# Kernel optimization log

Hardware: AMD Instinct MI355X
Metric: run time of the kernel (lower is better)

## Reference

```python
import jax, jax.numpy as jnp
import numpy as np

B, S, E, H, L, OUT = 128, 256, 300, 512, 2, 2


def _lstm_dir(x, mask, w_ih, w_hh, b, h0, c0, reverse):
    """One direction of one LSTM layer with length masking (packed-seq semantics).
    x: [B,S,D], mask: [B,S] bool (t < length). Returns (outputs [B,S,H], final h [B,H]).
    For reverse=True, scan runs t=S-1..0; state only updates once t < length, which
    exactly reproduces pack_padded_sequence reverse-direction behavior.
    """
    def step(carry, inp):
        h, c = carry
        xt, mt = inp  # [B,D], [B]
        z = xt @ w_ih.T + h @ w_hh.T + b  # [B,4H], torch gate order i,f,g,o
        i, f, g, o = jnp.split(z, 4, axis=-1)
        c_new = jax.nn.sigmoid(f) * c + jax.nn.sigmoid(i) * jnp.tanh(g)
        h_new = jax.nn.sigmoid(o) * jnp.tanh(c_new)
        m = mt[:, None]
        h = jnp.where(m, h_new, h)
        c = jnp.where(m, c_new, c)
        return (h, c), h
    (hT, _), hs = jax.lax.scan(step, (h0, c0), (jnp.swapaxes(x, 0, 1), mask.T), reverse=reverse)
    return jnp.swapaxes(hs, 0, 1), hT


def setup_inputs():
    key = jax.random.key(0)
    ks = iter(jax.random.split(key, 32))
    lengths = jax.random.randint(next(ks), (B,), 1, S + 1)
    x = jax.random.normal(next(ks), (B, S, E), jnp.float32)
    # module encodes per-sample lengths in input[:, -1, 0]
    x = x.at[:, -1, 0].set(lengths.astype(jnp.float32))
    k = 1.0 / np.sqrt(H)
    def u(shape):
        return jax.random.uniform(next(ks), shape, jnp.float32, -k, k)
    d = {"x": x}
    for l in range(L):
        din = E if l == 0 else 2 * H
        for suf in ("f", "r"):
            d[f"w_ih_l{l}_{suf}"] = u((4 * H, din))
            d[f"w_hh_l{l}_{suf}"] = u((4 * H, H))
            d[f"b_ih_l{l}_{suf}"] = u((4 * H,))
            d[f"b_hh_l{l}_{suf}"] = u((4 * H,))
    d["fc1_w"] = u((H, H))
    d["fc1_b"] = u((H,))
    d["fc_w"] = u((OUT, H))
    d["fc_b"] = u((OUT,))
    return d


def _forward(x, params):
    Bx, Sx = x.shape[0], x.shape[1]
    lengths = jnp.minimum(x[:, -1, 0].astype(jnp.int32), Sx)  # clamp(max=seq_len)
    mask = jnp.arange(Sx)[None, :] < lengths[:, None]  # [B,S]
    h0 = jnp.ones((Bx, H), x.dtype)  # module uses ones, not zeros
    c0 = jnp.ones((Bx, H), x.dtype)
    inp = x
    hT_r = None
    for l in range(L):
        (wif, whf, bif, bhf), (wir, whr, bir, bhr) = params[l]
        out_f, _ = _lstm_dir(inp, mask, wif, whf, bif + bhf, h0, c0, False)
        out_r, hT_r = _lstm_dir(inp, mask, wir, whr, bir + bhr, h0, c0, True)
        inp = jnp.concatenate([out_f, out_r], axis=-1)  # [B,S,2H]
    # ht[-1] == final hidden of reverse direction of last layer
    return hT_r


def reference(x, w_ih_l0_f, w_hh_l0_f, b_ih_l0_f, b_hh_l0_f,
              w_ih_l0_r, w_hh_l0_r, b_ih_l0_r, b_hh_l0_r,
              w_ih_l1_f, w_hh_l1_f, b_ih_l1_f, b_hh_l1_f,
              w_ih_l1_r, w_hh_l1_r, b_ih_l1_r, b_hh_l1_r,
              fc1_w, fc1_b, fc_w, fc_b):
    params = [((w_ih_l0_f, w_hh_l0_f, b_ih_l0_f, b_hh_l0_f),
               (w_ih_l0_r, w_hh_l0_r, b_ih_l0_r, b_hh_l0_r)),
              ((w_ih_l1_f, w_hh_l1_f, b_ih_l1_f, b_hh_l1_f),
               (w_ih_l1_r, w_hh_l1_r, b_ih_l1_r, b_hh_l1_r))]
    ht = _forward(x, params)  # [B,H]
    out = ht @ fc1_w.T + fc1_b  # fc1 (no activation in original)
    return out @ fc_w.T + fc_b  # [B,OUT]
```

## Files before the change

### kernel.cpp

```cpp
#include <hip/hip_runtime.h>

#define B_  128
#define S_  256
#define E_  300
#define EP_ 320
#define H_  512
#define G_  2048
#define D1_ 1024
#define G2_ 4096
#define FSLOT_ 4
#define FA_WORDS_ (4*FSLOT_*4*32*32)
#define FC_WORDS_ (2*FSLOT_*4*32*32)

typedef _Float16 f16;
typedef __attribute__((ext_vector_type(8))) _Float16 f16x8;
typedef __attribute__((ext_vector_type(4))) float    f32x4;
typedef unsigned long long u64;
typedef unsigned int u32;

__device__ __forceinline__ float sigf(float x){ return 1.f/(1.f + __expf(-x)); }
__device__ __forceinline__ float tanhf_(float x){
  float e = __expf(-2.f*fabsf(x));
  float t = (1.f - e)/(1.f + e);
  return x < 0.f ? -t : t;
}

__device__ __forceinline__ u64 aload64(const u64* p){
  return __hip_atomic_load((u64*)p, __ATOMIC_RELAXED, __HIP_MEMORY_SCOPE_AGENT);
}
__device__ __forceinline__ u32 aload32(const u32* p){
  return __hip_atomic_load((u32*)p, __ATOMIC_RELAXED, __HIP_MEMORY_SCOPE_AGENT);
}
__device__ __forceinline__ void astore32(u32* p, u32 v){
  __hip_atomic_store(p, v, __ATOMIC_RELAXED, __HIP_MEMORY_SCOPE_AGENT);
}
union H8 { u64 q[2]; f16x8 v; };
union FU { f16 f; unsigned short s; };


__global__ void k_f32_to_f16(const float* __restrict__ s, f16* __restrict__ d, int n){
  int i = blockIdx.x*blockDim.x + threadIdx.x;
  if (i < n) d[i] = (f16)s[i];
}

__global__ void k_pad_w(const float* __restrict__ s, f16* __restrict__ d, int rows, int ks, int kd){
  int i = blockIdx.x*blockDim.x + threadIdx.x;
  if (i >= rows*kd) return;
  int r = i/kd, k = i - r*kd;
  d[i] = (k < ks) ? (f16)s[(size_t)r*ks + k] : (f16)0.f;
}

__global__ void k_cast_x(const float* __restrict__ x, f16* __restrict__ xf){
  int i = blockIdx.x*blockDim.x + threadIdx.x;
  if (i >= S_*B_*EP_) return;
  int e = i % EP_; int rm = i / EP_;
  int m = rm % B_; int t = rm / B_;
  xf[i] = (e < E_) ? (f16)x[((size_t)m*S_ + t)*E_ + e] : (f16)0.f;
}

__global__ void k_bias(const float* __restrict__ a, const float* __restrict__ b,
                       float* __restrict__ d, int n){
  int i = blockIdx.x*blockDim.x + threadIdx.x;
  if (i < n) d[i] = a[i] + b[i];
}

__global__ void k_len(const float* __restrict__ x, int* __restrict__ len){
  int b = threadIdx.x;
  if (b < B_){
    int v = (int)x[((size_t)b*S_ + (S_-1))*E_];
    len[b] = v > S_ ? S_ : v;
  }
}

__global__ void k_zero(u32* __restrict__ p, int n){
  int i = blockIdx.x*blockDim.x + threadIdx.x;
  if (i < n) p[i] = 0u;
}

__global__ void k_init(f16* hxA, f16* hx1, float* cstate){
  int i = blockIdx.x*blockDim.x + threadIdx.x;
  if (i < B_*H_){
    hxA[i] = (f16)1.f;
    hxA[2*B_*H_ + i] = (f16)1.f;
    hx1[i] = (f16)1.f;
    cstate[i] = 1.f;
  }
}


__global__ __launch_bounds__(256) void k_gemm_bt(
    const f16* __restrict__ A, const f16* __restrict__ Bm,
    f16* __restrict__ C, const float* __restrict__ bias,
    int M, int N, int K)
{
  __shared__ f16 As[128*32];
  __shared__ f16 Bs[128*32];
  const int m0 = blockIdx.x*128, n0 = blockIdx.y*128;
  const int tid = threadIdx.x;
  const int w = tid>>6, lane = tid&63, quad = lane>>4, l16 = lane&15;
  const int wm = (w&1)*64, wn = (w>>1)*64;
  const int srow = w*32 + (lane>>2);
  const int scol = (lane&3)*8;
  const f16* Ap  = A  + (size_t)(m0 + srow)*K + scol;
  const f16* Bp  = Bm + (size_t)(n0 + srow)*K + scol;
  const f16* Ap2 = Ap + (size_t)16*K;
  const f16* Bp2 = Bp + (size_t)16*K;
  f16* ldsA  = &As[(w*32)*32];
  f16* ldsA2 = &As[(w*32+16)*32];
  f16* ldsB  = &Bs[(w*32)*32];
  f16* ldsB2 = &Bs[(w*32+16)*32];
  f32x4 z4 = {0.f,0.f,0.f,0.f};
  f32x4 acc[4][4];
#pragma unroll
  for (int mi = 0; mi < 4; ++mi)
#pragma unroll
    for (int ni = 0; ni < 4; ++ni) acc[mi][ni] = z4;

  for (int k0 = 0; k0 < K; k0 += 32){
    __builtin_amdgcn_global_load_lds(
        (const __attribute__((address_space(1))) void*)(Ap + k0),
        (__attribute__((address_space(3))) void*)ldsA, 16, 0, 0);
    __builtin_amdgcn_global_load_lds(
        (const __attribute__((address_space(1))) void*)(Ap2 + k0),
        (__attribute__((address_space(3))) void*)ldsA2, 16, 0, 0);
    __builtin_amdgcn_global_load_lds(
        (const __attribute__((address_space(1))) void*)(Bp + k0),
        (__attribute__((address_space(3))) void*)ldsB, 16, 0, 0);
    __builtin_amdgcn_global_load_lds(
        (const __attribute__((address_space(1))) void*)(Bp2 + k0),
        (__attribute__((address_space(3))) void*)ldsB2, 16, 0, 0);
    asm volatile("s_waitcnt vmcnt(0)" ::: "memory");
    __syncthreads();
    f16x8 a[4], b[4];
#pragma unroll
    for (int mi = 0; mi < 4; ++mi)
      a[mi] = *(const f16x8*)&As[(wm + mi*16 + l16)*32 + quad*8];
#pragma unroll
    for (int ni = 0; ni < 4; ++ni)
      b[ni] = *(const f16x8*)&Bs[(wn + ni*16 + l16)*32 + quad*8];
#pragma unroll
    for (int mi = 0; mi < 4; ++mi)
#pragma unroll
      for (int ni = 0; ni < 4; ++ni)
        acc[mi][ni] = __builtin_amdgcn_mfma_f32_16x16x32_f16(a[mi], b[ni], acc[mi][ni],0,0,0);
    __syncthreads();
  }
#pragma unroll
  for (int mi = 0; mi < 4; ++mi)
#pragma unroll
    for (int ni = 0; ni < 4; ++ni){
      int col = n0 + wn + ni*16 + l16;
      float bz = bias[col];
#pragma unroll
      for (int r = 0; r < 4; ++r){
        int row = m0 + wm + mi*16 + quad*4 + r;
        C[(size_t)row*N + col] = (f16)(acc[mi][ni][r] + bz);
      }
    }
}


__global__ __launch_bounds__(256, 1) void k_phaseA(
    const float* __restrict__ x, const f16* __restrict__ xz,
    const f16* __restrict__ w0f, const f16* __restrict__ w0r,
    const f16* __restrict__ whf, const f16* __restrict__ whr,
    const float* __restrict__ bs0, const int* __restrict__ len,
    f16* __restrict__ hxA, f16* __restrict__ outcat,
    u32* __restrict__ flagsA)
{
  __shared__ f16 Wh[64*512];
  __shared__ f16 Wi[64*320];
  const int half = blockIdx.x, jb = blockIdx.y, dir = blockIdx.z;
  const f16* wih = dir ? w0r : w0f;
  const f16* whh = dir ? whr : whf;
  const float* bias = bs0 + dir*G_;
  f16* hx = hxA + (size_t)dir*(2*B_*H_);
  u32* fbase = flagsA + (size_t)(dir*2 + half)*(FSLOT_*4*32*32);
  const int tid = threadIdx.x;
  const int w = tid>>6, lane = tid&63, quad = lane>>4, l16 = lane&15;
  const int j0 = jb*16;
  const int m0 = half*64 + w*16;

  for (int u = tid; u < 4096; u += 256){
    int lrr = u>>6, uc = u&63;
    int g = lrr>>4, i = lrr&15;
    *(uint4*)&Wh[lrr*512 + (uc ^ (i&7))*8] =
        *(const uint4*)(whh + ((size_t)(g*H_ + j0 + i))*H_ + uc*8);
  }
  if (!xz){
    for (int u = tid; u < 2560; u += 256){
      int row = u/40, c = u - row*40;
      int g = row>>4, i = row&15;
      *(uint4*)&Wi[row*320 + (c ^ (i&7))*8] =
          *(const uint4*)(wih + ((size_t)(g*H_ + j0 + i))*EP_ + c*8);
    }
  }
  __syncthreads();

  const int j = j0 + l16;
  float bz[4], hprev[4], cpr[4]; int lm[4];
#pragma unroll
  for (int g = 0; g < 4; ++g) bz[g] = bias[g*H_ + j];
#pragma unroll
  for (int r = 0; r < 4; ++r){ hprev[r] = 1.f; cpr[r] = 1.f; lm[r] = len[m0 + quad*4 + r]; }
  const size_t xrowbase = (size_t)(m0 + l16)*S_;

  if (xz){
    for (int s = 0; s < S_; ++s){
      const int t = dir ? (S_-1-s) : s;

      const f16* zr = xz + ((size_t)t*B_)*G2_ + dir*G_;
      float zvv[4][4];
#pragma unroll
      for (int g = 0; g < 4; ++g)
#pragma unroll
        for (int r = 0; r < 4; ++r)
          zvv[g][r] = (float)zr[(size_t)(m0 + quad*4 + r)*G2_ + g*H_ + j];

      if (s > 0){
        const u32* fp = fbase + ((size_t)((s-1)&(FSLOT_-1))*4 + w)*32*32;
        const u32 expv = (u32)s;
        for (;;){
          u32 v = aload32(fp + (size_t)(lane & 31)*32);
          if (__ballot(v == expv) == ~0ull) break;
        }
        asm volatile("" ::: "memory");
      }

      const int par = s & 1;
      const u64* hap = (const u64*)(hx + (size_t)par*(B_*H_) + (size_t)(m0 + l16)*H_);
      f32x4 z4 = {0.f,0.f,0.f,0.f};
      f32x4 acc[4] = {z4,z4,z4,z4};
      u64 hq[32];
#pragma unroll
      for (int kb = 0; kb < 16; ++kb){
        hq[2*kb]   = aload64(hap + kb*8 + quad*2);
        hq[2*kb+1] = aload64(hap + kb*8 + quad*2 + 1);
      }
#pragma unroll
      for (int kb = 0; kb < 16; ++kb){
        H8 ha;
        ha.q[0] = hq[2*kb];
        ha.q[1] = hq[2*kb+1];
        int uq = kb*4 + quad;
#pragma unroll
        for (int g = 0; g < 4; ++g){
          f16x8 b = *(const f16x8*)&Wh[(g*16+l16)*512 + ((uq ^ (l16&7)))*8];
          acc[g] = __builtin_amdgcn_mfma_f32_16x16x32_f16(ha.v, b, acc[g],0,0,0);
        }
      }

      f16* hn = hx + (size_t)(1-par)*(B_*H_);
#pragma unroll
      for (int r = 0; r < 4; ++r){
        int m = m0 + quad*4 + r;
        float zi = acc[0][r] + zvv[0][r];
        float zf = acc[1][r] + zvv[1][r];
        float zg = acc[2][r] + zvv[2][r];
        float zo = acc[3][r] + zvv[3][r];
        float ig = sigf(zi), fg = sigf(zf), gg = tanhf_(zg), og = sigf(zo);
        float cnew = fg*cpr[r] + ig*gg;
        float hnew = og*tanhf_(cnew);
        bool mk = t < lm[r];
        float hsel = mk ? hnew : hprev[r];
        cpr[r] = mk ? cnew : cpr[r];
        hprev[r] = hsel;
        FU cv; cv.f = (f16)hsel;
        int other = __shfl_down((int)cv.s, 1);
        if ((l16 & 1) == 0)
          astore32((u32*)(hn + (size_t)m*H_ + j), (u32)cv.s | ((u32)other << 16));
      }
      asm volatile("s_waitcnt vmcnt(0)" ::: "memory");
      if (lane == 0)
        astore32(fbase + (((size_t)(s&(FSLOT_-1))*4 + w)*32 + jb)*32, (u32)(s+1));

#pragma unroll
      for (int r = 0; r < 4; ++r){
        int m = m0 + quad*4 + r;
        FU cv; cv.f = (f16)hprev[r];
        int other = __shfl_down((int)cv.s, 1);
        if ((l16 & 1) == 0)
          *(u32*)(outcat + ((size_t)t*B_ + m)*D1_ + dir*H_ + j) = (u32)cv.s | ((u32)other << 16);
      }
    }
    return;
  }

  float4 xA[9], xB[9]; float xT[8];
  {
    const int t0 = dir ? (S_-1) : 0;
    const float* xr = x + (xrowbase + t0)*E_;
#pragma unroll
    for (int kb = 0; kb < 9; ++kb){
      xA[kb] = *(const float4*)(xr + kb*32 + quad*8);
      xB[kb] = *(const float4*)(xr + kb*32 + quad*8 + 4);
    }
    int kbase = 288 + quad*8;
#pragma unroll
    for (int e2 = 0; e2 < 8; ++e2)
      xT[e2] = (kbase + e2 < E_) ? xr[kbase + e2] : 0.f;
  }

  for (int s = 0; s < S_; ++s){
    const int t = dir ? (S_-1-s) : s;
    f32x4 z4 = {0.f,0.f,0.f,0.f};
    f32x4 acc[4] = {z4,z4,z4,z4};

#pragma unroll
    for (int kb = 0; kb < 9; ++kb){
      f16x8 a;
      a[0]=(f16)xA[kb].x; a[1]=(f16)xA[kb].y; a[2]=(f16)xA[kb].z; a[3]=(f16)xA[kb].w;
      a[4]=(f16)xB[kb].x; a[5]=(f16)xB[kb].y; a[6]=(f16)xB[kb].z; a[7]=(f16)xB[kb].w;
      int c = (kb*4 + quad) ^ (l16 & 7);
#pragma unroll
      for (int g = 0; g < 4; ++g){
        f16x8 b = *(const f16x8*)&Wi[(g*16+l16)*320 + c*8];
        acc[g] = __builtin_amdgcn_mfma_f32_16x16x32_f16(a, b, acc[g],0,0,0);
      }
    }
    {
      f16x8 a;
#pragma unroll
      for (int e2 = 0; e2 < 8; ++e2) a[e2] = (f16)xT[e2];
      int c = (36 + quad) ^ (l16 & 7);
#pragma unroll
      for (int g = 0; g < 4; ++g){
        f16x8 b = *(const f16x8*)&Wi[(g*16+l16)*320 + c*8];
        acc[g] = __builtin_amdgcn_mfma_f32_16x16x32_f16(a, b, acc[g],0,0,0);
      }
    }

    if (s+1 < S_){
      const int tn = dir ? (S_-2-s) : (s+1);
      const float* xr = x + (xrowbase + tn)*E_;
#pragma unroll
      for (int kb = 0; kb < 9; ++kb){
        xA[kb] = *(const float4*)(xr + kb*32 + quad*8);
        xB[kb] = *(const float4*)(xr + kb*32 + quad*8 + 4);
      }
      int kbase = 288 + quad*8;
#pragma unroll
      for (int e2 = 0; e2 < 8; ++e2)
        xT[e2] = (kbase + e2 < E_) ? xr[kbase + e2] : 0.f;
    }

    if (s > 0){
      const u32* fp = fbase + ((size_t)((s-1)&(FSLOT_-1))*4 + w)*32*32;
      const u32 expv = (u32)s;
      for (;;){
        u32 v = aload32(fp + (size_t)(lane & 31)*32);
        if (__ballot(v == expv) == ~0ull) break;
      }
      asm volatile("" ::: "memory");
    }

    const int par = s & 1;
    const u64* hap = (const u64*)(hx + (size_t)par*(B_*H_) + (size_t)(m0 + l16)*H_);
    u64 hq[32];
#pragma unroll
    for (int kb = 0; kb < 16; ++kb){
      hq[2*kb]   = aload64(hap + kb*8 + quad*2);
      hq[2*kb+1] = aload64(hap + kb*8 + quad*2 + 1);
    }
#pragma unroll
    for (int kb = 0; kb < 16; ++kb){
      H8 ha;
      ha.q[0] = hq[2*kb];
      ha.q[1] = hq[2*kb+1];
      int uq = kb*4 + quad;
#pragma unroll
      for (int g = 0; g < 4; ++g){
        f16x8 b = *(const f16x8*)&Wh[(g*16+l16)*512 + ((uq ^ (l16&7)))*8];
        acc[g] = __builtin_amdgcn_mfma_f32_16x16x32_f16(ha.v, b, acc[g],0,0,0);
      }
    }

    f16* hn = hx + (size_t)(1-par)*(B_*H_);
#pragma unroll
    for (int r = 0; r < 4; ++r){
      int m = m0 + quad*4 + r;
      float zi = acc[0][r] + bz[0];
      float zf = acc[1][r] + bz[1];
      float zg = acc[2][r] + bz[2];
      float zo = acc[3][r] + bz[3];
      float ig = sigf(zi), fg = sigf(zf), gg = tanhf_(zg), og = sigf(zo);
      float cnew = fg*cpr[r] + ig*gg;
      float hnew = og*tanhf_(cnew);
      bool mk = t < lm[r];
      float hsel = mk ? hnew : hprev[r];
      cpr[r] = mk ? cnew : cpr[r];
      hprev[r] = hsel;
      FU cv; cv.f = (f16)hsel;
      int other = __shfl_down((int)cv.s, 1);
      if ((l16 & 1) == 0)
        astore32((u32*)(hn + (size_t)m*H_ + j), (u32)cv.s | ((u32)other << 16));
    }
    asm volatile("s_waitcnt vmcnt(0)" ::: "memory");
    if (lane == 0)
      astore32(fbase + (((size_t)(s&(FSLOT_-1))*4 + w)*32 + jb)*32, (u32)(s+1));

#pragma unroll
    for (int r = 0; r < 4; ++r){
      int m = m0 + quad*4 + r;
      FU cv; cv.f = (f16)hprev[r];
      int other = __shfl_down((int)cv.s, 1);
      if ((l16 & 1) == 0)
        *(u32*)(outcat + ((size_t)t*B_ + m)*D1_ + dir*H_ + j) = (u32)cv.s | ((u32)other << 16);
    }
  }
}


__global__ __launch_bounds__(256, 1) void k_phaseCrec(
    const f16* __restrict__ Z1c, const f16* __restrict__ w1h,
    const int* __restrict__ len,
    f16* __restrict__ hx1, float* __restrict__ cstate, float* __restrict__ h1f,
    u32* __restrict__ flagsC, int s0, int CH)
{
  __shared__ f16 Wh[64*512];
  const int half = blockIdx.x, jb = blockIdx.y;
  u32* fbase = flagsC + (size_t)half*(FSLOT_*4*32*32);
  const int tid = threadIdx.x;
  const int w = tid>>6, lane = tid&63, quad = lane>>4, l16 = lane&15;
  const int j0 = jb*16;
  const int m0 = half*64 + w*16;

  for (int u = tid; u < 4096; u += 256){
    int lrr = u>>6, uc = u&63;
    int g = lrr>>4, i = lrr&15;
    *(uint4*)&Wh[lrr*512 + (uc ^ (i&7))*8] =
        *(const uint4*)(w1h + ((size_t)(g*H_ + j0 + i))*H_ + uc*8);
  }
  __syncthreads();

  const int j = j0 + l16;
  float hprev[4], cpr[4]; int lm[4];
#pragma unroll
  for (int r = 0; r < 4; ++r){
    int m = m0 + quad*4 + r;
    lm[r] = len[m];
    cpr[r] = cstate[(size_t)m*H_ + j];
    hprev[r] = (float)hx1[(size_t)(s0 & 1)*(B_*H_) + (size_t)m*H_ + j];
  }

  for (int sl = 0; sl < CH; ++sl){
    const int s = s0 + sl;
    const int t = S_-1-s;
    const int zrow = CH-1-sl;

    float zv[4][4];
#pragma unroll
    for (int g = 0; g < 4; ++g)
#pragma unroll
      for (int r = 0; r < 4; ++r)
        zv[g][r] = (float)Z1c[((size_t)zrow*B_ + m0 + quad*4 + r)*G_ + g*H_ + j];

    if (s > 0){
      const u32* fp = fbase + ((size_t)((s-1)&(FSLOT_-1))*4 + w)*32*32;
      const u32 expv = (u32)s;
      for (;;){
        u32 v = aload32(fp + (size_t)(lane & 31)*32);
        if (__ballot(v == expv) == ~0ull) break;
      }
      asm volatile("" ::: "memory");
    }

    const int par = s & 1;
    const u64* hap = (const u64*)(hx1 + (size_t)par*(B_*H_) + (size_t)(m0 + l16)*H_);
    f32x4 z4 = {0.f,0.f,0.f,0.f};
    f32x4 acc[4] = {z4,z4,z4,z4};
    u64 hq[32];
#pragma unroll
    for (int kb = 0; kb < 16; ++kb){
      hq[2*kb]   = aload64(hap + kb*8 + quad*2);
      hq[2*kb+1] = aload64(hap + kb*8 + quad*2 + 1);
    }
#pragma unroll
    for (int kb = 0; kb < 16; ++kb){
      H8 ha;
      ha.q[0] = hq[2*kb];
      ha.q[1] = hq[2*kb+1];
      int uq = kb*4 + quad;
#pragma unroll
      for (int g = 0; g < 4; ++g){
        f16x8 b = *(const f16x8*)&Wh[(g*16+l16)*512 + ((uq ^ (l16&7)))*8];
        acc[g] = __builtin_amdgcn_mfma_f32_16x16x32_f16(ha.v, b, acc[g],0,0,0);
      }
    }

    f16* hn = hx1 + (size_t)(1-par)*(B_*H_);
#pragma unroll
    for (int r = 0; r < 4; ++r){
      int m = m0 + quad*4 + r;
      float zi = acc[0][r] + zv[0][r];
      float zf = acc[1][r] + zv[1][r];
      float zg = acc[2][r] + zv[2][r];
      float zo = acc[3][r] + zv[3][r];
      float ig = sigf(zi), fg = sigf(zf), gg = tanhf_(zg), og = sigf(zo);
      float cnew = fg*cpr[r] + ig*gg;
      float hnew = og*tanhf_(cnew);
      bool mk = t < lm[r];
      float hsel = mk ? hnew : hprev[r];
      cpr[r] = mk ? cnew : cpr[r];
      hprev[r] = hsel;
      FU cv; cv.f = (f16)hsel;
      int other = __shfl_down((int)cv.s, 1);
      if ((l16 & 1) == 0)
        astore32((u32*)(hn + (size_t)m*H_ + j), (u32)cv.s | ((u32)other << 16));
    }
    asm volatile("s_waitcnt vmcnt(0)" ::: "memory");
    if (lane == 0)
      astore32(fbase + (((size_t)(s&(FSLOT_-1))*4 + w)*32 + jb)*32, (u32)(s+1));

    if (t == 0){
#pragma unroll
      for (int r = 0; r < 4; ++r)
        h1f[(size_t)(m0 + quad*4 + r)*H_ + j] = hprev[r];
    }
  }

#pragma unroll
  for (int r = 0; r < 4; ++r)
    cstate[(size_t)(m0 + quad*4 + r)*H_ + j] = cpr[r];
}


__global__ void k_fold(const float* __restrict__ fc1w, const float* __restrict__ fc1b,
                       const float* __restrict__ fcw,  const float* __restrict__ fcb,
                       float* __restrict__ Mf, float* __restrict__ bf){
  int i = blockIdx.x*blockDim.x + threadIdx.x;
  if (i >= 1024) return;
  int o = i >> 9, h = i & 511;
  float s = 0.f;
  for (int jj = 0; jj < 512; ++jj) s += fcw[o*512 + jj] * fc1w[jj*512 + h];
  Mf[o*512 + h] = s;
  if (h == 0){
    float sb = fcb[o];
    for (int jj = 0; jj < 512; ++jj) sb += fcw[o*512 + jj] * fc1b[jj];
    bf[o] = sb;
  }
}

__global__ void k_final(const float* __restrict__ h1f, const float* __restrict__ Mf,
                        const float* __restrict__ bf, float* __restrict__ out){
  int i = threadIdx.x;
  if (i >= 256) return;
  int b = i >> 1, o = i & 1;
  float s = bf[o];
  const float* hp = h1f + (size_t)b*512;
  const float* mp = Mf + (size_t)o*512;
  for (int h = 0; h < 512; ++h) s += hp[h]*mp[h];
  out[b*2 + o] = s;
}


extern "C" void kernel_launch(void* const* d_in, const int* in_sizes, int n_in,
                              void* d_out, int out_size, void* d_ws, size_t ws_size,
                              hipStream_t stream)
{
  const float* x     = (const float*)d_in[0];
  const float* wih0f = (const float*)d_in[1];
  const float* whh0f = (const float*)d_in[2];
  const float* bih0f = (const float*)d_in[3];
  const float* bhh0f = (const float*)d_in[4];
  const float* wih0r = (const float*)d_in[5];
  const float* whh0r = (const float*)d_in[6];
  const float* bih0r = (const float*)d_in[7];
  const float* bhh0r = (const float*)d_in[8];
  const float* wih1r = (const float*)d_in[13];
  const float* whh1r = (const float*)d_in[14];
  const float* bih1r = (const float*)d_in[15];
  const float* bhh1r = (const float*)d_in[16];
  const float* fc1w  = (const float*)d_in[17];
  const float* fc1b  = (const float*)d_in[18];
  const float* fcw   = (const float*)d_in[19];
  const float* fcb   = (const float*)d_in[20];
  float* out = (float*)d_out;

  char* p = (char*)d_ws;
  auto alloc = [&](size_t bytes)->char*{
    char* r = p; p += (bytes + 255) & ~(size_t)255; return r;
  };
  f16* w0fp   = (f16*)alloc((size_t)G_*EP_*2);
  f16* w0rp   = (f16*)alloc((size_t)G_*EP_*2);
  f16* whf    = (f16*)alloc((size_t)G_*H_*2);
  f16* whr    = (f16*)alloc((size_t)G_*H_*2);
  f16* w1i    = (f16*)alloc((size_t)G_*D1_*2);
  f16* w1h    = (f16*)alloc((size_t)G_*H_*2);
  float* bs0  = (float*)alloc((size_t)2*G_*4);
  float* bs1r = (float*)alloc(G_*4);
  int*   len  = (int*)alloc(B_*4);
  f16* outcat = (f16*)alloc((size_t)S_*B_*D1_*2);
  f16* hxA    = (f16*)alloc((size_t)2*2*B_*H_*2);
  f16* hx1    = (f16*)alloc((size_t)2*B_*H_*2);
  float* cstate=(float*)alloc((size_t)B_*H_*4);
  float* h1f  = (float*)alloc((size_t)B_*H_*4);
  float* Mf   = (float*)alloc(2*512*4);
  float* bf   = (float*)alloc(256);
  u32* flagsA = (u32*)alloc((size_t)FA_WORDS_*4);
  u32* flagsC = (u32*)alloc((size_t)FC_WORDS_*4);
  size_t used = (size_t)(p - (char*)d_ws);

  const size_t XZ_BYTES = (size_t)S_*B_*G2_*2;
  const size_t XF_BYTES = (size_t)S_*B_*EP_*2;
  f16* Xz = nullptr; f16* xf = nullptr; f16* Z1c; int CH;
  if (used + XZ_BYTES + XF_BYTES + 512 <= ws_size){
    Xz  = (f16*)alloc(XZ_BYTES);
    xf  = (f16*)alloc(XF_BYTES);
    Z1c = Xz;
    CH  = 256;
  } else {
    CH = 8;
    for (int c = 256; c >= 8; c >>= 1){
      if (used + (size_t)c*B_*G_*2 <= ws_size){ CH = c; break; }
    }
    Z1c = (f16*)alloc((size_t)CH*B_*G_*2);
  }
  const int NC = S_/CH;

  int n;
  n = G_*EP_; k_pad_w<<<(n+255)/256, 256, 0, stream>>>(wih0f, w0fp, G_, E_, EP_);
              k_pad_w<<<(n+255)/256, 256, 0, stream>>>(wih0r, w0rp, G_, E_, EP_);
  n = G_*H_;  k_f32_to_f16<<<(n+255)/256,256,0,stream>>>(whh0f, whf, n);
              k_f32_to_f16<<<(n+255)/256,256,0,stream>>>(whh0r, whr, n);
              k_f32_to_f16<<<(n+255)/256,256,0,stream>>>(whh1r, w1h, n);
  n = G_*D1_; k_f32_to_f16<<<(n+255)/256,256,0,stream>>>(wih1r, w1i, n);
  k_bias<<<8,256,0,stream>>>(bih0f, bhh0f, bs0, G_);
  k_bias<<<8,256,0,stream>>>(bih0r, bhh0r, bs0 + G_, G_);
  k_bias<<<8,256,0,stream>>>(bih1r, bhh1r, bs1r, G_);
  k_len<<<1,128,0,stream>>>(x, len);
  k_init<<<(B_*H_+255)/256,256,0,stream>>>(hxA, hx1, cstate);
  k_zero<<<(FA_WORDS_+255)/256,256,0,stream>>>(flagsA, FA_WORDS_);
  k_zero<<<(FC_WORDS_+255)/256,256,0,stream>>>(flagsC, FC_WORDS_);
  k_fold<<<4,256,0,stream>>>(fc1w, fc1b, fcw, fcb, Mf, bf);

  if (Xz){
    n = S_*B_*EP_;
    k_cast_x<<<(n+255)/256, 256, 0, stream>>>(x, xf);
    k_gemm_bt<<<dim3(S_*B_/128, G2_/128), 256, 0, stream>>>(
        xf, w0fp, Xz, bs0, S_*B_, G2_, EP_);
  }

  k_phaseA<<<dim3(2,32,2), 256, 0, stream>>>(
      x, Xz, w0fp, w0rp, whf, whr, bs0, len, hxA, outcat, flagsA);

  for (int cc = 0; cc < NC; ++cc){
    int t0 = S_ - (cc+1)*CH;
    k_gemm_bt<<<dim3(CH, 16), 256, 0, stream>>>(
        outcat + (size_t)t0*B_*D1_, w1i, Z1c, bs1r, CH*B_, G_, D1_);
    k_phaseCrec<<<dim3(2,32), 256, 0, stream>>>(
        Z1c, w1h, len, hx1, cstate, h1f, flagsC, cc*CH, CH);
  }

  k_final<<<1,256,0,stream>>>(h1f, Mf, bf, out);
}
```

Baseline: 3.971 ms.

## Chunk layer-0 input projection per direction so recurrence fits smaller workspace

Replaces the single combined forward/reverse input-projection GEMM with separate per-direction GEMMs over time chunks sized to the available workspace. A new recurrent kernel consumes each chunk and persists cell and hidden state between launches, so the precomputed-projection path can run even when the full 256-step buffer does not fit. The aim is to avoid falling back to the slower kernel that recomputes the input projection inside the recurrence. In exchange it adds more launches, per-chunk state reload and store, and reloads of recurrent weights into LDS for each chunk.

```diff
diff --git a/kernel.cpp b/kernel.cpp
--- a/kernel.cpp
+++ b/kernel.cpp
@@ -7,7 +7,6 @@
 #define H_  512
 #define G_  2048
 #define D1_ 1024
-#define G2_ 4096
 #define FSLOT_ 4
 #define FA_WORDS_ (4*FSLOT_*4*32*32)
 #define FC_WORDS_ (2*FSLOT_*4*32*32)
@@ -77,13 +76,15 @@
   if (i < n) p[i] = 0u;
 }
 
-__global__ void k_init(f16* hxA, f16* hx1, float* cstate){
+__global__ void k_init(f16* hxA, f16* hx1, float* cstate, float* cstateA){
   int i = blockIdx.x*blockDim.x + threadIdx.x;
   if (i < B_*H_){
     hxA[i] = (f16)1.f;
     hxA[2*B_*H_ + i] = (f16)1.f;
     hx1[i] = (f16)1.f;
     cstate[i] = 1.f;
+    cstateA[i] = 1.f;
+    cstateA[B_*H_ + i] = 1.f;
   }
 }
 
@@ -160,8 +161,132 @@
 }
 
 
+__global__ __launch_bounds__(256, 1) void k_phaseA_xz(
+    const f16* __restrict__ Xzf, const f16* __restrict__ Xzr,
+    const f16* __restrict__ whf, const f16* __restrict__ whr,
+    const int* __restrict__ len,
+    f16* __restrict__ hxA, float* __restrict__ cstateA,
+    f16* __restrict__ outcat, u32* __restrict__ flagsA,
+    int s0, int CHA)
+{
+  __shared__ f16 Wh[64*512];
+  const int half = blockIdx.x, jb = blockIdx.y, dir = blockIdx.z;
+  const f16* whh = dir ? whr : whf;
+  const f16* Xz  = dir ? Xzr : Xzf;
+  f16* hx = hxA + (size_t)dir*(2*B_*H_);
+  float* cst = cstateA + (size_t)dir*(B_*H_);
+  u32* fbase = flagsA + (size_t)(dir*2 + half)*(FSLOT_*4*32*32);
+  const int tid = threadIdx.x;
+  const int w = tid>>6, lane = tid&63, quad = lane>>4, l16 = lane&15;
+  const int j0 = jb*16;
+  const int m0 = half*64 + w*16;
+
+  for (int u = tid; u < 4096; u += 256){
+    int lrr = u>>6, uc = u&63;
+    int g = lrr>>4, i = lrr&15;
+    *(uint4*)&Wh[lrr*512 + (uc ^ (i&7))*8] =
+        *(const uint4*)(whh + ((size_t)(g*H_ + j0 + i))*H_ + uc*8);
+  }
+  __syncthreads();
+
+  const int j = j0 + l16;
+  float hprev[4], cpr[4]; int lm[4];
+#pragma unroll
+  for (int r = 0; r < 4; ++r){
+    int m = m0 + quad*4 + r;
+    lm[r] = len[m];
+    cpr[r] = cst[(size_t)m*H_ + j];
+    hprev[r] = (float)hx[(size_t)(s0 & 1)*(B_*H_) + (size_t)m*H_ + j];
+  }
+
+  for (int sl = 0; sl < CHA; ++sl){
+    const int s = s0 + sl;
+    const int t = dir ? (S_-1-s) : s;
+    const int zrow = dir ? (CHA-1-sl) : sl;
+
+    const f16* zr = Xz + ((size_t)zrow*B_)*G_;
+    float zvv[4][4];
+#pragma unroll
+    for (int g = 0; g < 4; ++g)
+#pragma unroll
+      for (int r = 0; r < 4; ++r)
+        zvv[g][r] = (float)zr[(size_t)(m0 + quad*4 + r)*G_ + g*H_ + j];
+
+    if (s > 0){
+      const u32* fp = fbase + ((size_t)((s-1)&(FSLOT_-1))*4 + w)*32*32;
+      const u32 expv = (u32)s;
+      for (;;){
+        u32 v = aload32(fp + (size_t)(lane & 31)*32);
+        if (__ballot(v == expv) == ~0ull) break;
+      }
+      asm volatile("" ::: "memory");
+    }
+
+    const int par = s & 1;
+    const u64* hap = (const u64*)(hx + (size_t)par*(B_*H_) + (size_t)(m0 + l16)*H_);
+    f32x4 z4 = {0.f,0.f,0.f,0.f};
+    f32x4 acc[4] = {z4,z4,z4,z4};
+    u64 hq[32];
+#pragma unroll
+    for (int kb = 0; kb < 16; ++kb){
+      hq[2*kb]   = aload64(hap + kb*8 + quad*2);
+      hq[2*kb+1] = aload64(hap + kb*8 + quad*2 + 1);
+    }
+#pragma unroll
+    for (int kb = 0; kb < 16; ++kb){
+      H8 ha;
+      ha.q[0] = hq[2*kb];
+      ha.q[1] = hq[2*kb+1];
+      int uq = kb*4 + quad;
+#pragma unroll
+      for (int g = 0; g < 4; ++g){
+        f16x8 b = *(const f16x8*)&Wh[(g*16+l16)*512 + ((uq ^ (l16&7)))*8];
+        acc[g] = __builtin_amdgcn_mfma_f32_16x16x32_f16(ha.v, b, acc[g],0,0,0);
+      }
+    }
+
+    f16* hn = hx + (size_t)(1-par)*(B_*H_);
+#pragma unroll
+    for (int r = 0; r < 4; ++r){
+      int m = m0 + quad*4 + r;
+      float zi = acc[0][r] + zvv[0][r];
+      float zf = acc[1][r] + zvv[1][r];
+      float zg = acc[2][r] + zvv[2][r];
+      float zo = acc[3][r] + zvv[3][r];
+      float ig = sigf(zi), fg = sigf(zf), gg = tanhf_(zg), og = sigf(zo);
+      float cnew = fg*cpr[r] + ig*gg;
+      float hnew = og*tanhf_(cnew);
+      bool mk = t < lm[r];
+      float hsel = mk ? hnew : hprev[r];
+      cpr[r] = mk ? cnew : cpr[r];
+      hprev[r] = hsel;
+      FU cv; cv.f = (f16)hsel;
+      int other = __shfl_down((int)cv.s, 1);
+      if ((l16 & 1) == 0)
+        astore32((u32*)(hn + (size_t)m*H_ + j), (u32)cv.s | ((u32)other << 16));
+    }
+    asm volatile("s_waitcnt vmcnt(0)" ::: "memory");
+    if (lane == 0)
+      astore32(fbase + (((size_t)(s&(FSLOT_-1))*4 + w)*32 + jb)*32, (u32)(s+1));
+
+#pragma unroll
+    for (int r = 0; r < 4; ++r){
+      int m = m0 + quad*4 + r;
+      FU cv; cv.f = (f16)hprev[r];
+      int other = __shfl_down((int)cv.s, 1);
+      if ((l16 & 1) == 0)
+        *(u32*)(outcat + ((size_t)t*B_ + m)*D1_ + dir*H_ + j) = (u32)cv.s | ((u32)other << 16);
+    }
+  }
+
+#pragma unroll
+  for (int r = 0; r < 4; ++r)
+    cst[(size_t)(m0 + quad*4 + r)*H_ + j] = cpr[r];
+}
+
+
 __global__ __launch_bounds__(256, 1) void k_phaseA(
-    const float* __restrict__ x, const f16* __restrict__ xz,
+    const float* __restrict__ x,
     const f16* __restrict__ w0f, const f16* __restrict__ w0r,
     const f16* __restrict__ whf, const f16* __restrict__ whr,
     const float* __restrict__ bs0, const int* __restrict__ len,
@@ -187,13 +312,11 @@
     *(uint4*)&Wh[lrr*512 + (uc ^ (i&7))*8] =
         *(const uint4*)(whh + ((size_t)(g*H_ + j0 + i))*H_ + uc*8);
   }
-  if (!xz){
-    for (int u = tid; u < 2560; u += 256){
-      int row = u/40, c = u - row*40;
-      int g = row>>4, i = row&15;
-      *(uint4*)&Wi[row*320 + (c ^ (i&7))*8] =
-          *(const uint4*)(wih + ((size_t)(g*H_ + j0 + i))*EP_ + c*8);
-    }
+  for (int u = tid; u < 2560; u += 256){
+    int row = u/40, c = u - row*40;
+    int g = row>>4, i = row&15;
+    *(uint4*)&Wi[row*320 + (c ^ (i&7))*8] =
+        *(const uint4*)(wih + ((size_t)(g*H_ + j0 + i))*EP_ + c*8);
   }
   __syncthreads();
 
@@ -204,87 +327,6 @@
 #pragma unroll
   for (int r = 0; r < 4; ++r){ hprev[r] = 1.f; cpr[r] = 1.f; lm[r] = len[m0 + quad*4 + r]; }
   const size_t xrowbase = (size_t)(m0 + l16)*S_;
-
-  if (xz){
-    for (int s = 0; s < S_; ++s){
-      const int t = dir ? (S_-1-s) : s;
-
-      const f16* zr = xz + ((size_t)t*B_)*G2_ + dir*G_;
-      float zvv[4][4];
-#pragma unroll
-      for (int g = 0; g < 4; ++g)
-#pragma unroll
-        for (int r = 0; r < 4; ++r)
-          zvv[g][r] = (float)zr[(size_t)(m0 + quad*4 + r)*G2_ + g*H_ + j];
-
-      if (s > 0){
-        const u32* fp = fbase + ((size_t)((s-1)&(FSLOT_-1))*4 + w)*32*32;
-        const u32 expv = (u32)s;
-        for (;;){
-          u32 v = aload32(fp + (size_t)(lane & 31)*32);
-          if (__ballot(v == expv) == ~0ull) break;
-        }
-        asm volatile("" ::: "memory");
-      }
-
-      const int par = s & 1;
-      const u64* hap = (const u64*)(hx + (size_t)par*(B_*H_) + (size_t)(m0 + l16)*H_);
-      f32x4 z4 = {0.f,0.f,0.f,0.f};
-      f32x4 acc[4] = {z4,z4,z4,z4};
-      u64 hq[32];
-#pragma unroll
-      for (int kb = 0; kb < 16; ++kb){
-        hq[2*kb]   = aload64(hap + kb*8 + quad*2);
-        hq[2*kb+1] = aload64(hap + kb*8 + quad*2 + 1);
-      }
-#pragma unroll
-      for (int kb = 0; kb < 16; ++kb){
-        H8 ha;
-        ha.q[0] = hq[2*kb];
-        ha.q[1] = hq[2*kb+1];
-        int uq = kb*4 + quad;
-#pragma unroll
-        for (int g = 0; g < 4; ++g){
-          f16x8 b = *(const f16x8*)&Wh[(g*16+l16)*512 + ((uq ^ (l16&7)))*8];
-          acc[g] = __builtin_amdgcn_mfma_f32_16x16x32_f16(ha.v, b, acc[g],0,0,0);
-        }
-      }
-
-      f16* hn = hx + (size_t)(1-par)*(B_*H_);
-#pragma unroll
-      for (int r = 0; r < 4; ++r){
-        int m = m0 + quad*4 + r;
-        float zi = acc[0][r] + zvv[0][r];
-        float zf = acc[1][r] + zvv[1][r];
-        float zg = acc[2][r] + zvv[2][r];
-        float zo = acc[3][r] + zvv[3][r];
-        float ig = sigf(zi), fg = sigf(zf), gg = tanhf_(zg), og = sigf(zo);
-        float cnew = fg*cpr[r] + ig*gg;
-        float hnew = og*tanhf_(cnew);
-        bool mk = t < lm[r];
-        float hsel = mk ? hnew : hprev[r];
-        cpr[r] = mk ? cnew : cpr[r];
-        hprev[r] = hsel;
-        FU cv; cv.f = (f16)hsel;
-        int other = __shfl_down((int)cv.s, 1);
-        if ((l16 & 1) == 0)
-          astore32((u32*)(hn + (size_t)m*H_ + j), (u32)cv.s | ((u32)other << 16));
-      }
-      asm volatile("s_waitcnt vmcnt(0)" ::: "memory");
-      if (lane == 0)
-        astore32(fbase + (((size_t)(s&(FSLOT_-1))*4 + w)*32 + jb)*32, (u32)(s+1));
-
-#pragma unroll
-      for (int r = 0; r < 4; ++r){
-        int m = m0 + quad*4 + r;
-        FU cv; cv.f = (f16)hprev[r];
-        int other = __shfl_down((int)cv.s, 1);
-        if ((l16 & 1) == 0)
-          *(u32*)(outcat + ((size_t)t*B_ + m)*D1_ + dir*H_ + j) = (u32)cv.s | ((u32)other << 16);
-      }
-    }
-    return;
-  }
 
   float4 xA[9], xB[9]; float xT[8];
   {
@@ -593,7 +635,8 @@
   f16* outcat = (f16*)alloc((size_t)S_*B_*D1_*2);
   f16* hxA    = (f16*)alloc((size_t)2*2*B_*H_*2);
   f16* hx1    = (f16*)alloc((size_t)2*B_*H_*2);
-  float* cstate=(float*)alloc((size_t)B_*H_*4);
+  float* cstate =(float*)alloc((size_t)B_*H_*4);
+  float* cstateA=(float*)alloc((size_t)2*B_*H_*4);
   float* h1f  = (float*)alloc((size_t)B_*H_*4);
   float* Mf   = (float*)alloc(2*512*4);
   float* bf   = (float*)alloc(256);
@@ -601,20 +644,26 @@
   u32* flagsC = (u32*)alloc((size_t)FC_WORDS_*4);
   size_t used = (size_t)(p - (char*)d_ws);
 
-  const size_t XZ_BYTES = (size_t)S_*B_*G2_*2;
-  const size_t XF_BYTES = (size_t)S_*B_*EP_*2;
-  f16* Xz = nullptr; f16* xf = nullptr; f16* Z1c; int CH;
-  if (used + XZ_BYTES + XF_BYTES + 512 <= ws_size){
-    Xz  = (f16*)alloc(XZ_BYTES);
-    xf  = (f16*)alloc(XF_BYTES);
-    Z1c = Xz;
-    CH  = 256;
+  const size_t XFB = (size_t)S_*B_*EP_*2;
+  const size_t CHUNK1 = (size_t)B_*G_*2;
+  f16* xf = nullptr; f16* Xzf = nullptr; f16* Xzr = nullptr;
+  int CHA = 0;
+  for (int c = 256; c >= 16; c >>= 1){
+    if (used + XFB + 2*(size_t)c*CHUNK1 + 1024 <= ws_size){ CHA = c; break; }
+  }
+  f16* Z1c; int CH;
+  if (CHA){
+    xf  = (f16*)alloc(XFB);
+    Xzf = (f16*)alloc((size_t)CHA*CHUNK1);
+    Xzr = (f16*)alloc((size_t)CHA*CHUNK1);
+    Z1c = Xzf;
+    CH  = (2*CHA > 256) ? 256 : 2*CHA;
   } else {
     CH = 8;
     for (int c = 256; c >= 8; c >>= 1){
-      if (used + (size_t)c*B_*G_*2 <= ws_size){ CH = c; break; }
-    }
-    Z1c = (f16*)alloc((size_t)CH*B_*G_*2);
+      if (used + (size_t)c*CHUNK1 <= ws_size){ CH = c; break; }
+    }
+    Z1c = (f16*)alloc((size_t)CH*CHUNK1);
   }
   const int NC = S_/CH;
 
@@ -629,20 +678,30 @@
   k_bias<<<8,256,0,stream>>>(bih0r, bhh0r, bs0 + G_, G_);
   k_bias<<<8,256,0,stream>>>(bih1r, bhh1r, bs1r, G_);
   k_len<<<1,128,0,stream>>>(x, len);
-  k_init<<<(B_*H_+255)/256,256,0,stream>>>(hxA, hx1, cstate);
+  k_init<<<(B_*H_+255)/256,256,0,stream>>>(hxA, hx1, cstate, cstateA);
   k_zero<<<(FA_WORDS_+255)/256,256,0,stream>>>(flagsA, FA_WORDS_);
   k_zero<<<(FC_WORDS_+255)/256,256,0,stream>>>(flagsC, FC_WORDS_);
   k_fold<<<4,256,0,stream>>>(fc1w, fc1b, fcw, fcb, Mf, bf);
 
-  if (Xz){
+  if (CHA){
     n = S_*B_*EP_;
     k_cast_x<<<(n+255)/256, 256, 0, stream>>>(x, xf);
-    k_gemm_bt<<<dim3(S_*B_/128, G2_/128), 256, 0, stream>>>(
-        xf, w0fp, Xz, bs0, S_*B_, G2_, EP_);
-  }
-
-  k_phaseA<<<dim3(2,32,2), 256, 0, stream>>>(
-      x, Xz, w0fp, w0rp, whf, whr, bs0, len, hxA, outcat, flagsA);
+    const int NCA = S_/CHA;
+    for (int ca = 0; ca < NCA; ++ca){
+      int s0  = ca*CHA;
+      int t0f = s0;
+      int t0r = S_ - CHA - s0;
+      k_gemm_bt<<<dim3(CHA, G_/128), 256, 0, stream>>>(
+          xf + (size_t)t0f*B_*EP_, w0fp, Xzf, bs0,      CHA*B_, G_, EP_);
+      k_gemm_bt<<<dim3(CHA, G_/128), 256, 0, stream>>>(
+          xf + (size_t)t0r*B_*EP_, w0rp, Xzr, bs0 + G_, CHA*B_, G_, EP_);
+      k_phaseA_xz<<<dim3(2,32,2), 256, 0, stream>>>(
+          Xzf, Xzr, whf, whr, len, hxA, cstateA, outcat, flagsA, s0, CHA);
+    }
+  } else {
+    k_phaseA<<<dim3(2,32,2), 256, 0, stream>>>(
+        x, w0fp, w0rp, whf, whr, bs0, len, hxA, outcat, flagsA);
+  }
 
   for (int cc = 0; cc < NC; ++cc){
     int t0 = S_ - (cc+1)*CH;
```

Result: faster. 3.685 ms (-7.2%).
